# Performance work log

Hardware: AMD Instinct MI355X
Metric: run time of the kernel (lower is better)

The kernel has to match this reference:

```python
import jax, jax.numpy as jnp
import numpy as np

D_MODEL = 1024
NUM_HEAD = 16
D_HEAD = 64
SEQ = 1024
MEM = 1024
BATCH = 4
LN_EPS = 1e-5


def _rel_shift(x):
    # x: [i, j, b, n] -- Transformer-XL relative shift trick
    i, j, b, n = x.shape
    zero_pad = jnp.zeros((i, 1, b, n), dtype=x.dtype)
    x_padded = jnp.concatenate([zero_pad, x], axis=1).reshape(j + 1, i, b, n)
    return x_padded[1:].reshape(i, j, b, n)


def setup_inputs() -> dict:
    key = jax.random.key(0)
    ks = jax.random.split(key, 8)
    w_scale = 1.0 / np.sqrt(D_MODEL)  # keep activations O(1)
    total = MEM + SEQ
    return {
        "x": jax.random.normal(ks[0], (SEQ, BATCH, D_MODEL), jnp.float32),
        "memory": jax.random.normal(ks[1], (MEM, BATCH, D_MODEL), jnp.float32),
        "pos_emb": jax.random.normal(ks[2], (total, BATCH, D_MODEL), jnp.float32),
        "pos_bias_u": jax.random.normal(ks[3], (NUM_HEAD, D_HEAD), jnp.float32) * 0.02,
        "pos_bias_v": jax.random.normal(ks[4], (NUM_HEAD, D_HEAD), jnp.float32) * 0.02,
        "W_qkv": jax.random.normal(ks[5], (3 * NUM_HEAD * D_HEAD, D_MODEL), jnp.float32) * w_scale,
        "W_rel": jax.random.normal(ks[6], (NUM_HEAD * D_HEAD, D_MODEL), jnp.float32) * w_scale,
        "W_o": jax.random.normal(ks[7], (D_MODEL, NUM_HEAD * D_HEAD), jnp.float32) * w_scale,
        "ln_gamma": jnp.ones((D_MODEL,), jnp.float32),
        "ln_beta": jnp.zeros((D_MODEL,), jnp.float32),
    }


def reference(x, memory, pos_emb, pos_bias_u, pos_bias_v, W_qkv, W_rel, W_o, ln_gamma, ln_beta):
    seq_len = x.shape[0]
    c = jnp.concatenate([memory, x], axis=0)        # [T, B, D]
    T, B = c.shape[0], c.shape[1]
    n, d = pos_bias_u.shape
    scale = 1.0 / np.sqrt(d)

    heads = c @ W_qkv.T                              # [T, B, 3*n*d]
    q, k, v = jnp.split(heads, 3, axis=-1)
    q = q.reshape(T, B, n, d)[-seq_len:]             # [S, B, n, d]
    k = k.reshape(T, B, n, d)                        # [T, B, n, d]
    v = v.reshape(T, B, n, d)
    r = (pos_emb @ W_rel.T).reshape(T, B, n, d)      # [T, B, n, d]

    AC = jnp.einsum('ibnd,jbnd->ijbn', q + pos_bias_u, k)
    BD = _rel_shift(jnp.einsum('ibnd,jbnd->ijbn', q + pos_bias_v, r))
    attn_score = (AC + BD) * scale                   # [S, T, B, n]
    attn_prob = jax.nn.softmax(attn_score, axis=1)   # softmax over key dim (dropout = eval identity)

    attn_vec = jnp.einsum('ijbn,jbnd->ibnd', attn_prob, v).reshape(seq_len, B, n * d)
    attn_out = attn_vec @ W_o.T                      # [S, B, D]

    y = x + attn_out
    mu = jnp.mean(y, axis=-1, keepdims=True)
    var = jnp.mean(jnp.square(y - mu), axis=-1, keepdims=True)
    return ln_gamma * (y - mu) / jnp.sqrt(var + LN_EPS) + ln_beta
```

## Files before the change

### kernel.cpp

```cpp
#include <hip/hip_runtime.h>

#define S_ 1024
#define M_ 1024
#define T_ 2048
#define B_ 4
#define H_ 16
#define DM_ 1024
#define DH_ 64

typedef __attribute__((ext_vector_type(8))) short s16x8;
typedef __attribute__((ext_vector_type(16))) float f32x16;

__device__ __forceinline__ unsigned short f2b(float x){
  unsigned int u = __float_as_uint(x);
  u = (u + 0x7fffu + ((u>>16)&1u)) >> 16;
  return (unsigned short)u;
}
__device__ __forceinline__ float b2f(unsigned short h){
  return __uint_as_float(((unsigned int)h)<<16);
}
__device__ __forceinline__ uint4 pack8(const float* v){
  uint4 o;
  o.x = (unsigned)f2b(v[0]) | ((unsigned)f2b(v[1])<<16);
  o.y = (unsigned)f2b(v[2]) | ((unsigned)f2b(v[3])<<16);
  o.z = (unsigned)f2b(v[4]) | ((unsigned)f2b(v[5])<<16);
  o.w = (unsigned)f2b(v[6]) | ((unsigned)f2b(v[7])<<16);
  return o;
}
__device__ __forceinline__ void glds16(const unsigned short* g, unsigned short* l){
  __builtin_amdgcn_global_load_lds((const __attribute__((address_space(1))) void*)g,
                                   (__attribute__((address_space(3))) void*)l, 16, 0, 0);
}

#define BAR_L()   asm volatile("s_waitcnt lgkmcnt(0)\ns_barrier" ::: "memory")
#define BAR_VL()  asm volatile("s_waitcnt vmcnt(0) lgkmcnt(0)\ns_barrier" ::: "memory")
#define BAR_V6L() asm volatile("s_waitcnt vmcnt(6) lgkmcnt(0)\ns_barrier" ::: "memory")

__global__ __launch_bounds__(256) void cast_all(
    const float* __restrict__ mem, const float* __restrict__ x,
    const float* __restrict__ pos, const float* __restrict__ wqkv,
    const float* __restrict__ wrel, const float* __restrict__ wo,
    unsigned short* __restrict__ c16, unsigned short* __restrict__ pos16,
    unsigned short* __restrict__ wq16, unsigned short* __restrict__ wr16,
    unsigned short* __restrict__ wo16)
{
  int u = blockIdx.x*256 + threadIdx.x;
  const float* s; unsigned short* d;
  if (u < 1048576)      { s = (u < 524288) ? mem + (size_t)u*8 : x + (size_t)(u-524288)*8;
                          d = c16 + (size_t)u*8; }
  else if (u < 2097152) { int v = u - 1048576; s = pos  + (size_t)v*8; d = pos16 + (size_t)v*8; }
  else if (u < 2490368) { int v = u - 2097152; s = wqkv + (size_t)v*8; d = wq16  + (size_t)v*8; }
  else if (u < 2621440) { int v = u - 2490368; s = wrel + (size_t)v*8; d = wr16  + (size_t)v*8; }
  else                  { int v = u - 2621440; s = wo   + (size_t)v*8; d = wo16  + (size_t)v*8; }
  float4 x0 = *(const float4*)s;
  float4 x1 = *(const float4*)(s+4);
  float f[8] = {x0.x,x0.y,x0.z,x0.w,x1.x,x1.y,x1.z,x1.w};
  *(uint4*)d = pack8(f);
}

__global__ __launch_bounds__(256) void gemm_nt(const unsigned short* __restrict__ A,
    const unsigned short* __restrict__ Bw, void* __restrict__ Cout,
    const float* __restrict__ res, int Ntot, int K, int mode)
{
  __shared__ __align__(16) unsigned short a_s[128*64];
  __shared__ __align__(16) unsigned short b_s[128*64];
  const int tid = threadIdx.x;
  const int lane = tid & 63, wave = tid >> 6;
  const int wr = wave >> 1, wc = wave & 1;
  const long m0 = (long)blockIdx.y * 128, n0 = (long)blockIdx.x * 128;
  f32x16 acc[2][2];
  for (int qa=0;qa<2;qa++) for(int qb=0;qb<2;qb++) for (int e=0;e<16;e++) acc[qa][qb][e]=0.f;
  int srow[4], scol[4];
  for (int c = 0; c < 4; c++) {
    int ch = c*256 + tid;
    srow[c] = ch >> 3;
    scol[c] = (((ch & 7) ^ (srow[c] & 7))) * 8;
  }
  for (int k0 = 0; k0 < K; k0 += 64) {
    for (int c = 0; c < 4; c++) {
      int ch = c*256 + tid;
      glds16(&A[(size_t)(m0+srow[c])*K + k0 + scol[c]], &a_s[ch*8]);
      glds16(&Bw[(size_t)(n0+srow[c])*K + k0 + scol[c]], &b_s[ch*8]);
    }
    __syncthreads();
    for (int ks = 0; ks < 4; ks++) {
      const int kb = ks*2 + (lane>>5);
      s16x8 af[2], bf[2];
      for (int q = 0; q < 2; q++) {
        int ra = wr*64 + q*32 + (lane&31);
        int rb = wc*64 + q*32 + (lane&31);
        af[q] = *(const s16x8*)&a_s[ra*64 + ((kb ^ (ra&7))<<3)];
        bf[q] = *(const s16x8*)&b_s[rb*64 + ((kb ^ (rb&7))<<3)];
      }
      for (int qr=0;qr<2;qr++)
        for (int qc2=0;qc2<2;qc2++)
          acc[qr][qc2] = __builtin_amdgcn_mfma_f32_32x32x16_bf16(af[qr], bf[qc2], acc[qr][qc2], 0,0,0);
    }
    __syncthreads();
  }
  for (int qr=0;qr<2;qr++)
    for (int qc2=0;qc2<2;qc2++)
      for (int e=0;e<16;e++){
        long row = m0 + wr*64 + qr*32 + (e&3) + 8*(e>>2) + 4*(lane>>5);
        long col = n0 + wc*64 + qc2*32 + (lane&31);
        size_t o = (size_t)row*Ntot + col;
        if (mode == 0) ((unsigned short*)Cout)[o] = f2b(acc[qr][qc2][e]);
        else           ((float*)Cout)[o] = acc[qr][qc2][e] + res[o];
      }
}

__global__ __launch_bounds__(256) void scatter_quv(const unsigned short* __restrict__ qkvo,
   const float* __restrict__ u, const float* __restrict__ v,
   unsigned short* __restrict__ QU, unsigned short* __restrict__ QV)
{
  int gid = blockIdx.x*256 + threadIdx.x;
  int d0 = (gid & 7) * 8;
  int i  = (gid >> 3) & (S_-1);
  int bh = gid >> 13;
  int b = bh >> 4, h = bh & 15;
  size_t src = (size_t)((M_+i)*B_ + b)*3072 + h*64 + d0;
  uint4 q8 = *(const uint4*)&qkvo[src];
  float f[8];
  f[0]=b2f(q8.x&0xffff); f[1]=b2f(q8.x>>16); f[2]=b2f(q8.y&0xffff); f[3]=b2f(q8.y>>16);
  f[4]=b2f(q8.z&0xffff); f[5]=b2f(q8.z>>16); f[6]=b2f(q8.w&0xffff); f[7]=b2f(q8.w>>16);
  float fu[8], fv[8];
  for (int e=0;e<8;e++){ fu[e] = f[e] + u[h*64+d0+e]; fv[e] = f[e] + v[h*64+d0+e]; }
  size_t dst = ((size_t)bh*S_ + i)*64 + d0;
  *(uint4*)&QU[dst] = pack8(fu);
  *(uint4*)&QV[dst] = pack8(fv);
}

__global__ __launch_bounds__(256) void scatter_vt(const unsigned short* __restrict__ qkvo,
    unsigned short* __restrict__ VT)
{
  __shared__ __align__(16) unsigned short v_s[64*72];
  const int tid = threadIdx.x;
  const int bh = blockIdx.x, b = bh>>4, h = bh&15;
  const int t0 = blockIdx.y*64;
  const unsigned short* Vg = qkvo + (size_t)b*3072 + 2048 + h*64;
  for (int c=0;c<2;c++){
    int ch = c*256 + tid;
    int r = ch>>3, off = (ch&7)*8;
    *(uint4*)&v_s[r*72+off] = *(const uint4*)&Vg[(size_t)(t0+r)*12288 + off];
  }
  __syncthreads();
  for (int c=0;c<2;c++){
    int ch = c*256 + tid;
    int d = ch>>3, toff = (ch&7)*8;
    unsigned short vals[8];
    for (int e=0;e<8;e++) vals[e] = v_s[(toff+e)*72 + d];
    uint4 pk;
    pk.x = (unsigned)vals[0] | ((unsigned)vals[1]<<16);
    pk.y = (unsigned)vals[2] | ((unsigned)vals[3]<<16);
    pk.z = (unsigned)vals[4] | ((unsigned)vals[5]<<16);
    pk.w = (unsigned)vals[6] | ((unsigned)vals[7]<<16);
    *(uint4*)&VT[((size_t)bh*64 + d)*T_ + t0 + toff] = pk;
  }
}

__global__ __launch_bounds__(256,2) void flash_attn4(
    const unsigned short* __restrict__ QU, const unsigned short* __restrict__ QV,
    const unsigned short* __restrict__ qkvo, const unsigned short* __restrict__ VT,
    const unsigned short* __restrict__ relo, unsigned short* __restrict__ AV)
{
  __shared__ __align__(16) unsigned short qv_s[65*72];
  __shared__ __align__(16) unsigned short k_s [64*64];
  __shared__ __align__(16) unsigned short vt_s[64*64];
  __shared__ __align__(16) unsigned short rg_s[128*64];
  __shared__ __align__(16) unsigned short p_s [64*64];
  __shared__ float l_s[64];

  const int tid = threadIdx.x, lane = tid&63, wave = tid>>6;
  const int bh = blockIdx.x, b = bh>>4, h = bh&15;
  const int i0 = blockIdx.y*64;
  const int qr = wave>>1, qc = wave&1;
  const int hi = lane>>5, ll = lane&31;
  const unsigned short* QUb = QU + (size_t)bh*S_*DH_;
  const unsigned short* QVb = QV + (size_t)bh*S_*DH_;
  const unsigned short* Kg  = qkvo + (size_t)b*3072 + 1024 + h*64;
  const unsigned short* VTb = VT + (size_t)bh*64*T_;
  const unsigned short* Rg  = relo + (size_t)b*1024 + h*64;

  const int s0r = tid>>3,        s0c = (((tid&7)       ^ (s0r&7)))*8;
  const int s1r = (256+tid)>>3,  s1c = ((((256+tid)&7) ^ (s1r&7)))*8;

  glds16(&Kg [(size_t)(0+s0r)*12288 + s0c], &k_s[(size_t)tid*8]);
  glds16(&Kg [(size_t)(0+s1r)*12288 + s1c], &k_s[(size_t)(256+tid)*8]);
  {
    const int wb0 = 0 - i0 + 960;
    for (int c=0;c<4;c++){
      int ch = c*256+tid; int rr = ch>>3, off = ch&7;
      int t = wb0 + rr; t = t < 0 ? 0 : (t > T_-1 ? T_-1 : t);
      int sc = ((off ^ (rr&7)))*8;
      glds16(&Rg[(size_t)t*4096 + sc], &rg_s[(size_t)ch*8]);
    }
  }
  for (int c=0;c<2;c++){
    int ch = c*256+tid; int row = ch>>3, off=(ch&7);
    *(uint4*)&p_s[row*64 + ((off ^ (row&7))<<3)] = *(const uint4*)&QUb[(size_t)(i0+row)*64 + off*8];
    *(uint4*)&qv_s[row*72+off*8] = *(const uint4*)&QVb[(size_t)(i0+row)*64 + off*8];
  }
  if (tid < 8) {
    int rr = i0 + 64; if (rr > S_-1) rr = S_-1;
    *(uint4*)&qv_s[64*72 + tid*8] = *(const uint4*)&QVb[(size_t)rr*64 + tid*8];
  }
  BAR_L();

  s16x8 qur0, qur1, qur2, qur3;
  s16x8 qv00, qv01, qv02, qv03;
  {
    const int rq = qr*32 + ll;
    qur0 = *(const s16x8*)&p_s[rq*64 + (((0*2+hi) ^ (rq&7))<<3)];
    qur1 = *(const s16x8*)&p_s[rq*64 + (((1*2+hi) ^ (rq&7))<<3)];
    qur2 = *(const s16x8*)&p_s[rq*64 + (((2*2+hi) ^ (rq&7))<<3)];
    qur3 = *(const s16x8*)&p_s[rq*64 + (((3*2+hi) ^ (rq&7))<<3)];
    const int ro = rq*72 + hi*8;
    qv00 = *(const s16x8*)&qv_s[ro +  0];
    qv01 = *(const s16x8*)&qv_s[ro + 16];
    qv02 = *(const s16x8*)&qv_s[ro + 32];
    qv03 = *(const s16x8*)&qv_s[ro + 48];
  }
  BAR_VL();

  s16x8 ones;
  for (int e=0;e<8;e++) ones[e] = (short)0x3F80;

  f32x16 acc_o, acc_l;
  for (int e=0;e<16;e++){ acc_o[e]=0.f; acc_l[e]=0.f; }

  const int col = qc*32 + ll;
  const int cbase = (qc - qr + 1) * 32;

  for (int j0 = 0; j0 < T_; j0 += 64) {
    const int jdmax = j0 + 63 - i0;
    const int jdmin = j0 - 63 - i0;
    const int cls = (jdmax <= 1024) ? 0 : ((jdmin >= 1026) ? 2 : 1);
    const int jn = j0 + 64;

    if (j0) BAR_VL();

    glds16(&VTb[(size_t)s0r*T_ + j0 + s0c], &vt_s[(size_t)tid*8]);
    glds16(&VTb[(size_t)s1r*T_ + j0 + s1c], &vt_s[(size_t)(256+tid)*8]);

    s16x8 av0, av1, av2, av3;
    if (cls == 2) {
      const int ro1 = (qr*32+ll+1)*72 + hi*8;
      av0 = *(const s16x8*)&qv_s[ro1 +  0];
      av1 = *(const s16x8*)&qv_s[ro1 + 16];
      av2 = *(const s16x8*)&qv_s[ro1 + 32];
      av3 = *(const s16x8*)&qv_s[ro1 + 48];
    } else {
      av0 = qv00; av1 = qv01; av2 = qv02; av3 = qv03;
    }

    f32x16 gacc0, gacc1;
    for (int e=0;e<16;e++){ gacc0[e]=0.f; gacc1[e]=0.f; }
    __builtin_amdgcn_s_setprio(1);
#define BANDK(KS, AV) { \
      int kb = KS*2 + hi; \
      { int br = cbase + ll; \
        s16x8 bb = *(const s16x8*)&rg_s[br*64 + ((kb ^ (br&7))<<3)]; \
        gacc0 = __builtin_amdgcn_mfma_f32_32x32x16_bf16(AV, bb, gacc0, 0,0,0); } \
      { int br = cbase + 32 + ll; \
        s16x8 bb = *(const s16x8*)&rg_s[br*64 + ((kb ^ (br&7))<<3)]; \
        gacc1 = __builtin_amdgcn_mfma_f32_32x32x16_bf16(AV, bb, gacc1, 0,0,0); } }
    BANDK(0, av0) BANDK(1, av1) BANDK(2, av2) BANDK(3, av3)

    f32x16 acc;
    for (int e=0;e<16;e++) acc[e]=0.f;
#define ACK(KS, AU) { \
      int kb = KS*2 + hi; \
      int rbk = qc*32 + ll; \
      s16x8 bq = *(const s16x8*)&k_s[rbk*64 + ((kb ^ (rbk&7))<<3)]; \
      acc = __builtin_amdgcn_mfma_f32_32x32x16_bf16(AU, bq, acc, 0,0,0); }
    ACK(0, qur0) ACK(1, qur1) ACK(2, qur2) ACK(3, qur3)
    __builtin_amdgcn_s_setprio(0);
    BAR_L();

    if (jn < T_) {
      glds16(&Kg[(size_t)(jn+s0r)*12288 + s0c], &k_s[(size_t)tid*8]);
      glds16(&Kg[(size_t)(jn+s1r)*12288 + s1c], &k_s[(size_t)(256+tid)*8]);
      if (cls != 1) {
        const int jdmaxn = jn + 63 - i0;
        const int jdminn = jn - 63 - i0;
        const int clsn = (jdmaxn <= 1024) ? 0 : ((jdminn >= 1026) ? 2 : 1);
        const int wbn = (clsn == 2) ? (jn - i0 - 1089) : (jn - i0 + 960);
        for (int c=0;c<4;c++){
          int ch = c*256+tid; int rr = ch>>3, off = ch&7;
          int t = wbn + rr; t = t < 0 ? 0 : (t > T_-1 ? T_-1 : t);
          int sc = ((off ^ (rr&7)))*8;
          glds16(&Rg[(size_t)t*4096 + sc], &rg_s[(size_t)ch*8]);
        }
      }
    }

    for (int e=0;e<16;e++){
      int rm = 4*hi + (e&3) + 8*(e>>2);
      int r  = qr*32 + rm;
      int jd = j0 + col - (i0 + r);
      int tl = (ll + rm + 1) & 31;
      float sel = (tl > rm) ? gacc1[e] : gacc0[e];
      int li = ((((ll - rm + 31) & 31) | (hi<<5)) << 2);
      float bd = __uint_as_float((unsigned)__builtin_amdgcn_ds_bpermute(li, (int)__float_as_uint(sel)));
      if (jd == 1025) bd = 0.f;
      float p = __expf((acc[e] + bd) * 0.125f);
      if (!(cls == 1 && jd >= 1026))
        p_s[r*64 + (((col>>3) ^ (r&7))<<3) + (col&7)] = f2b(p);
    }

    if (cls == 1) {
      const int wb2 = j0 - i0 - 1089;
      for (int c=0;c<4;c++){
        int ch = c*256+tid; int rr = ch>>3, off = ch&7;
        int t = wb2 + rr; t = t < 0 ? 0 : (t > T_-1 ? T_-1 : t);
        int sc = ((off ^ (rr&7)))*8;
        glds16(&Rg[(size_t)t*4096 + sc], &rg_s[(size_t)ch*8]);
      }
      BAR_VL();
      f32x16 g2a, g2b;
      for (int e=0;e<16;e++){ g2a[e]=0.f; g2b[e]=0.f; }
      __builtin_amdgcn_s_setprio(1);
#define BANDW(KS) { \
        int kb = KS*2 + hi; \
        const int ro1 = (qr*32+ll+1)*72 + hi*8; \
        s16x8 a = *(const s16x8*)&qv_s[ro1 + KS*16]; \
        { int br = cbase + ll; \
          s16x8 bb = *(const s16x8*)&rg_s[br*64 + ((kb ^ (br&7))<<3)]; \
          g2a = __builtin_amdgcn_mfma_f32_32x32x16_bf16(a, bb, g2a, 0,0,0); } \
        { int br = cbase + 32 + ll; \
          s16x8 bb = *(const s16x8*)&rg_s[br*64 + ((kb ^ (br&7))<<3)]; \
          g2b = __builtin_amdgcn_mfma_f32_32x32x16_bf16(a, bb, g2b, 0,0,0); } }
      BANDW(0) BANDW(1) BANDW(2) BANDW(3)
      __builtin_amdgcn_s_setprio(0);
      for (int e=0;e<16;e++){
        int rm = 4*hi + (e&3) + 8*(e>>2);
        int r  = qr*32 + rm;
        int jd = j0 + col - (i0 + r);
        int tl = (ll + rm + 1) & 31;
        float sel = (tl > rm) ? g2b[e] : g2a[e];
        int li = ((((ll - rm + 31) & 31) | (hi<<5)) << 2);
        float bd = __uint_as_float((unsigned)__builtin_amdgcn_ds_bpermute(li, (int)__float_as_uint(sel)));
        float p = __expf((acc[e] + bd) * 0.125f);
        if (jd >= 1026)
          p_s[r*64 + (((col>>3) ^ (r&7))<<3) + (col&7)] = f2b(p);
      }
      BAR_L();
      if (jn < T_) {
        const int jdmaxn = jn + 63 - i0;
        const int jdminn = jn - 63 - i0;
        const int clsn = (jdmaxn <= 1024) ? 0 : ((jdminn >= 1026) ? 2 : 1);
        const int wbn = (clsn == 2) ? (jn - i0 - 1089) : (jn - i0 + 960);
        for (int c=0;c<4;c++){
          int ch = c*256+tid; int rr = ch>>3, off = ch&7;
          int t = wbn + rr; t = t < 0 ? 0 : (t > T_-1 ? T_-1 : t);
          int sc = ((off ^ (rr&7)))*8;
          glds16(&Rg[(size_t)t*4096 + sc], &rg_s[(size_t)ch*8]);
        }
      }
    }

    if (jn < T_) { BAR_V6L(); } else { BAR_VL(); }

    __builtin_amdgcn_s_setprio(1);
    for (int ks=0; ks<4; ks++){
      int kb = ks*2 + hi;
      int rv = qr*32 + ll, rbv = qc*32 + ll;
      s16x8 a  = *(const s16x8*)&p_s[rv*64 + ((kb ^ (rv&7))<<3)];
      s16x8 bv = *(const s16x8*)&vt_s[rbv*64 + ((kb ^ (rbv&7))<<3)];
      acc_o = __builtin_amdgcn_mfma_f32_32x32x16_bf16(a, bv, acc_o, 0,0,0);
      acc_l = __builtin_amdgcn_mfma_f32_32x32x16_bf16(a, ones, acc_l, 0,0,0);
    }
    __builtin_amdgcn_s_setprio(0);
  }

  if (qc == 0 && ll == 0) {
    for (int e=0;e<16;e++){
      int r = qr*32 + 4*hi + (e&3) + 8*(e>>2);
      l_s[r] = acc_l[e];
    }
  }
  BAR_L();
  for (int e=0;e<16;e++){
    int r = qr*32 + 4*hi + (e&3) + 8*(e>>2);
    float oo = acc_o[e] / l_s[r];
    AV[ ((size_t)(i0+r)*B_ + b)*(H_*DH_) + h*DH_ + col ] = f2b(oo);
  }
#undef BANDK
#undef ACK
#undef BANDW
}

__global__ __launch_bounds__(256) void ln_kernel(const float* __restrict__ y,
    const float* __restrict__ g, const float* __restrict__ be, float* __restrict__ o)
{
  __shared__ float red[8];
  int row = blockIdx.x, tid = threadIdx.x;
  const float* yr = y + (size_t)row*DM_;
  float v[4];
  for (int e=0;e<4;e++) v[e] = yr[tid + 256*e];
  float s = v[0]+v[1]+v[2]+v[3];
  for (int off=32; off>0; off>>=1) s += __shfl_down(s, off, 64);
  if ((tid&63)==0) red[tid>>6] = s;
  __syncthreads();
  if (tid==0) red[4] = red[0]+red[1]+red[2]+red[3];
  __syncthreads();
  float mu = red[4] * (1.f/DM_);
  __syncthreads();
  float q = 0.f;
  for (int e=0;e<4;e++){ float d = v[e]-mu; q += d*d; }
  for (int off=32; off>0; off>>=1) q += __shfl_down(q, off, 64);
  if ((tid&63)==0) red[tid>>6] = q;
  __syncthreads();
  if (tid==0) red[4] = red[0]+red[1]+red[2]+red[3];
  __syncthreads();
  float rstd = rsqrtf(red[4]*(1.f/DM_) + 1e-5f);
  for (int e=0;e<4;e++){
    int c = tid + 256*e;
    o[(size_t)row*DM_ + c] = g[c]*(v[e]-mu)*rstd + be[c];
  }
}

extern "C" void kernel_launch(void* const* d_in, const int* in_sizes, int n_in,
                              void* d_out, int out_size, void* d_ws, size_t ws_size,
                              hipStream_t stream)
{
  const float* x    = (const float*)d_in[0];
  const float* mem  = (const float*)d_in[1];
  const float* pos  = (const float*)d_in[2];
  const float* pbu  = (const float*)d_in[3];
  const float* pbv  = (const float*)d_in[4];
  const float* wqkv = (const float*)d_in[5];
  const float* wrel = (const float*)d_in[6];
  const float* wo   = (const float*)d_in[7];
  const float* gam  = (const float*)d_in[8];
  const float* bet  = (const float*)d_in[9];
  float* out = (float*)d_out;

  char* w = (char*)d_ws;
  unsigned short* qkvo  = (unsigned short*)(w + 0);
  unsigned short* relo  = (unsigned short*)(w + 50331648);
  unsigned short* wo16  = (unsigned short*)(w + 67108864);
  unsigned short* QUb   = (unsigned short*)(w + 69206016);
  unsigned short* QVb   = (unsigned short*)(w + 77594624);
  unsigned short* VT    = (unsigned short*)(w + 85983232);
  unsigned short* av16  = (unsigned short*)(w + 102760448);
  float*          yf    = (float*)(w + 111149056);
  unsigned short* c16   = (unsigned short*)(w + 127926272);
  unsigned short* pos16 = (unsigned short*)(w + 144703488);
  unsigned short* wq16  = (unsigned short*)(w + 161480704);
  unsigned short* wr16  = (unsigned short*)(w + 167772160);

  cast_all<<<10752, 256, 0, stream>>>(mem, x, pos, wqkv, wrel, wo,
                                      c16, pos16, wq16, wr16, wo16);

  gemm_nt<<<dim3(24,64), 256, 0, stream>>>(c16,   wq16, (void*)qkvo, nullptr, 3072, 1024, 0);
  gemm_nt<<<dim3(8,64),  256, 0, stream>>>(pos16, wr16, (void*)relo, nullptr, 1024, 1024, 0);

  scatter_quv<<<2048, 256, 0, stream>>>(qkvo, pbu, pbv, QUb, QVb);
  scatter_vt<<<dim3(64,32), 256, 0, stream>>>(qkvo, VT);

  flash_attn4<<<dim3(64,16), 256, 0, stream>>>(QUb, QVb, qkvo, VT, relo, av16);

  gemm_nt<<<dim3(8,32), 256, 0, stream>>>(av16, wo16, (void*)yf, x, 1024, 1024, 1);
  ln_kernel<<<4096, 256, 0, stream>>>(yf, gam, bet, out);
}
```

Measured before the change: 462.5 us.

## Double-buffer K and relative-position tiles in LDS to overlap prefetch

```diff
diff --git a/kernel.cpp b/kernel.cpp
--- a/kernel.cpp
+++ b/kernel.cpp
@@ -164,9 +164,9 @@
     const unsigned short* __restrict__ relo, unsigned short* __restrict__ AV)
 {
   __shared__ __align__(16) unsigned short qv_s[65*72];
-  __shared__ __align__(16) unsigned short k_s [64*64];
+  __shared__ __align__(16) unsigned short k_s [2][64*64];
   __shared__ __align__(16) unsigned short vt_s[64*64];
-  __shared__ __align__(16) unsigned short rg_s[128*64];
+  __shared__ __align__(16) unsigned short rg_s[2][128*64];
   __shared__ __align__(16) unsigned short p_s [64*64];
   __shared__ float l_s[64];
 
@@ -184,15 +184,14 @@
   const int s0r = tid>>3,        s0c = (((tid&7)       ^ (s0r&7)))*8;
   const int s1r = (256+tid)>>3,  s1c = ((((256+tid)&7) ^ (s1r&7)))*8;
 
-  glds16(&Kg [(size_t)(0+s0r)*12288 + s0c], &k_s[(size_t)tid*8]);
-  glds16(&Kg [(size_t)(0+s1r)*12288 + s1c], &k_s[(size_t)(256+tid)*8]);
+  glds16(&Kg [(size_t)(0+s0r)*12288 + s0c], &k_s[0][(size_t)tid*8]);
+  glds16(&Kg [(size_t)(0+s1r)*12288 + s1c], &k_s[0][(size_t)(256+tid)*8]);
   {
     const int wb0 = 0 - i0 + 960;
     for (int c=0;c<4;c++){
       int ch = c*256+tid; int rr = ch>>3, off = ch&7;
       int t = wb0 + rr; t = t < 0 ? 0 : (t > T_-1 ? T_-1 : t);
-      int sc = ((off ^ (rr&7)))*8;
-      glds16(&Rg[(size_t)t*4096 + sc], &rg_s[(size_t)ch*8]);
+      glds16(&Rg[(size_t)t*4096 + ((off ^ (rr&7)))*8], &rg_s[0][(size_t)ch*8]);
     }
   }
   for (int c=0;c<2;c++){
@@ -220,7 +219,6 @@
     qv02 = *(const s16x8*)&qv_s[ro + 32];
     qv03 = *(const s16x8*)&qv_s[ro + 48];
   }
-  BAR_VL();
 
   s16x8 ones;
   for (int e=0;e<8;e++) ones[e] = (short)0x3F80;
@@ -231,16 +229,34 @@
   const int col = qc*32 + ll;
   const int cbase = (qc - qr + 1) * 32;
 
+  int cur = 0;
   for (int j0 = 0; j0 < T_; j0 += 64) {
     const int jdmax = j0 + 63 - i0;
     const int jdmin = j0 - 63 - i0;
     const int cls = (jdmax <= 1024) ? 0 : ((jdmin >= 1026) ? 2 : 1);
     const int jn = j0 + 64;
-
-    if (j0) BAR_VL();
+    unsigned short* kc = &k_s[cur][0];
+    unsigned short* rc = &rg_s[cur][0];
+    unsigned short* kn = &k_s[cur^1][0];
+    unsigned short* rn = &rg_s[cur^1][0];
+
+    BAR_VL();
 
     glds16(&VTb[(size_t)s0r*T_ + j0 + s0c], &vt_s[(size_t)tid*8]);
     glds16(&VTb[(size_t)s1r*T_ + j0 + s1c], &vt_s[(size_t)(256+tid)*8]);
+    if (jn < T_) {
+      glds16(&Kg[(size_t)(jn+s0r)*12288 + s0c], &kn[(size_t)tid*8]);
+      glds16(&Kg[(size_t)(jn+s1r)*12288 + s1c], &kn[(size_t)(256+tid)*8]);
+      const int jdmaxn = jn + 63 - i0;
+      const int jdminn = jn - 63 - i0;
+      const int clsn = (jdmaxn <= 1024) ? 0 : ((jdminn >= 1026) ? 2 : 1);
+      const int wbn = (clsn == 2) ? (jn - i0 - 1089) : (jn - i0 + 960);
+      for (int c=0;c<4;c++){
+        int ch = c*256+tid; int rr = ch>>3, off = ch&7;
+        int t = wbn + rr; t = t < 0 ? 0 : (t > T_-1 ? T_-1 : t);
+        glds16(&Rg[(size_t)t*4096 + ((off ^ (rr&7)))*8], &rn[(size_t)ch*8]);
+      }
+    }
 
     s16x8 av0, av1, av2, av3;
     if (cls == 2) {
@@ -259,10 +275,10 @@
 #define BANDK(KS, AV) { \
       int kb = KS*2 + hi; \
       { int br = cbase + ll; \
-        s16x8 bb = *(const s16x8*)&rg_s[br*64 + ((kb ^ (br&7))<<3)]; \
+        s16x8 bb = *(const s16x8*)&rc[br*64 + ((kb ^ (br&7))<<3)]; \
         gacc0 = __builtin_amdgcn_mfma_f32_32x32x16_bf16(AV, bb, gacc0, 0,0,0); } \
       { int br = cbase + 32 + ll; \
-        s16x8 bb = *(const s16x8*)&rg_s[br*64 + ((kb ^ (br&7))<<3)]; \
+        s16x8 bb = *(const s16x8*)&rc[br*64 + ((kb ^ (br&7))<<3)]; \
         gacc1 = __builtin_amdgcn_mfma_f32_32x32x16_bf16(AV, bb, gacc1, 0,0,0); } }
     BANDK(0, av0) BANDK(1, av1) BANDK(2, av2) BANDK(3, av3)
 
@@ -271,28 +287,10 @@
 #define ACK(KS, AU) { \
       int kb = KS*2 + hi; \
       int rbk = qc*32 + ll; \
-      s16x8 bq = *(const s16x8*)&k_s[rbk*64 + ((kb ^ (rbk&7))<<3)]; \
+      s16x8 bq = *(const s16x8*)&kc[rbk*64 + ((kb ^ (rbk&7))<<3)]; \
       acc = __builtin_amdgcn_mfma_f32_32x32x16_bf16(AU, bq, acc, 0,0,0); }
     ACK(0, qur0) ACK(1, qur1) ACK(2, qur2) ACK(3, qur3)
     __builtin_amdgcn_s_setprio(0);
-    BAR_L();
-
-    if (jn < T_) {
-      glds16(&Kg[(size_t)(jn+s0r)*12288 + s0c], &k_s[(size_t)tid*8]);
-      glds16(&Kg[(size_t)(jn+s1r)*12288 + s1c], &k_s[(size_t)(256+tid)*8]);
-      if (cls != 1) {
-        const int jdmaxn = jn + 63 - i0;
-        const int jdminn = jn - 63 - i0;
-        const int clsn = (jdmaxn <= 1024) ? 0 : ((jdminn >= 1026) ? 2 : 1);
-        const int wbn = (clsn == 2) ? (jn - i0 - 1089) : (jn - i0 + 960);
-        for (int c=0;c<4;c++){
-          int ch = c*256+tid; int rr = ch>>3, off = ch&7;
-          int t = wbn + rr; t = t < 0 ? 0 : (t > T_-1 ? T_-1 : t);
-          int sc = ((off ^ (rr&7)))*8;
-          glds16(&Rg[(size_t)t*4096 + sc], &rg_s[(size_t)ch*8]);
-        }
-      }
-    }
 
     for (int e=0;e<16;e++){
       int rm = 4*hi + (e&3) + 8*(e>>2);
@@ -309,12 +307,12 @@
     }
 
     if (cls == 1) {
+      BAR_L();
       const int wb2 = j0 - i0 - 1089;
       for (int c=0;c<4;c++){
         int ch = c*256+tid; int rr = ch>>3, off = ch&7;
         int t = wb2 + rr; t = t < 0 ? 0 : (t > T_-1 ? T_-1 : t);
-        int sc = ((off ^ (rr&7)))*8;
-        glds16(&Rg[(size_t)t*4096 + sc], &rg_s[(size_t)ch*8]);
+        glds16(&Rg[(size_t)t*4096 + ((off ^ (rr&7)))*8], &rc[(size_t)ch*8]);
       }
       BAR_VL();
       f32x16 g2a, g2b;
@@ -325,10 +323,10 @@
         const int ro1 = (qr*32+ll+1)*72 + hi*8; \
         s16x8 a = *(const s16x8*)&qv_s[ro1 + KS*16]; \
         { int br = cbase + ll; \
-          s16x8 bb = *(const s16x8*)&rg_s[br*64 + ((kb ^ (br&7))<<3)]; \
+          s16x8 bb = *(const s16x8*)&rc[br*64 + ((kb ^ (br&7))<<3)]; \
           g2a = __builtin_amdgcn_mfma_f32_32x32x16_bf16(a, bb, g2a, 0,0,0); } \
         { int br = cbase + 32 + ll; \
-          s16x8 bb = *(const s16x8*)&rg_s[br*64 + ((kb ^ (br&7))<<3)]; \
+          s16x8 bb = *(const s16x8*)&rc[br*64 + ((kb ^ (br&7))<<3)]; \
           g2b = __builtin_amdgcn_mfma_f32_32x32x16_bf16(a, bb, g2b, 0,0,0); } }
       BANDW(0) BANDW(1) BANDW(2) BANDW(3)
       __builtin_amdgcn_s_setprio(0);
@@ -344,19 +342,6 @@
         if (jd >= 1026)
           p_s[r*64 + (((col>>3) ^ (r&7))<<3) + (col&7)] = f2b(p);
       }
-      BAR_L();
-      if (jn < T_) {
-        const int jdmaxn = jn + 63 - i0;
-        const int jdminn = jn - 63 - i0;
-        const int clsn = (jdmaxn <= 1024) ? 0 : ((jdminn >= 1026) ? 2 : 1);
-        const int wbn = (clsn == 2) ? (jn - i0 - 1089) : (jn - i0 + 960);
-        for (int c=0;c<4;c++){
-          int ch = c*256+tid; int rr = ch>>3, off = ch&7;
-          int t = wbn + rr; t = t < 0 ? 0 : (t > T_-1 ? T_-1 : t);
-          int sc = ((off ^ (rr&7)))*8;
-          glds16(&Rg[(size_t)t*4096 + sc], &rg_s[(size_t)ch*8]);
-        }
-      }
     }
 
     if (jn < T_) { BAR_V6L(); } else { BAR_VL(); }
@@ -371,6 +356,7 @@
       acc_l = __builtin_amdgcn_mfma_f32_32x32x16_bf16(a, ones, acc_l, 0,0,0);
     }
     __builtin_amdgcn_s_setprio(0);
+    cur ^= 1;
   }
 
   if (qc == 0 && ll == 0) {
```

After: 470.9 us. No clear change (+1.8%).
